# Kernel tuning notes

Hardware: AMD Instinct MI355X
Metric: run time of the kernel (lower is better)

The kernel has to match this reference:

```python
import jax, jax.numpy as jnp
import numpy as np

B, T, F, H, M = 64, 512, 32, 512, 20
O = (F + 2) * M  # (n_features + 2) * num_mixtures = 680


def _lstm_cell(x, h, c, w_ih, w_hh, b_ih, b_hh):
    # torch.nn.LSTMCell: gates ordered [i, f, g, o]
    gates = x @ w_ih.T + h @ w_hh.T + b_ih + b_hh
    i, f, g, o = jnp.split(gates, 4, axis=-1)
    i = jax.nn.sigmoid(i)
    f = jax.nn.sigmoid(f)
    g = jnp.tanh(g)
    o = jax.nn.sigmoid(o)
    c_new = f * c + i * g
    h_new = o * jnp.tanh(c_new)
    return h_new, c_new


def setup_inputs() -> dict:
    key = jax.random.key(0)
    ks = jax.random.split(key, 9)
    s1 = 1.0 / np.sqrt(H)  # torch LSTMCell init: U(-1/sqrt(hidden), 1/sqrt(hidden))
    s2 = 1.0 / np.sqrt(O)
    u = lambda k, shape, s: jax.random.uniform(k, shape, jnp.float32, -s, s)
    return {
        "data": jax.random.normal(ks[0], (B, T * F), jnp.float32),
        "W_ih1": u(ks[1], (4 * H, F), s1),
        "W_hh1": u(ks[2], (4 * H, H), s1),
        "b_ih1": u(ks[3], (4 * H,), s1),
        "b_hh1": u(ks[4], (4 * H,), s1),
        "W_ih2": u(ks[5], (4 * O, H), s2),
        "W_hh2": u(ks[6], (4 * O, O), s2),
        "b_ih2": u(ks[7], (4 * O,), s2),
        "b_hh2": u(ks[8], (4 * O,), s2),
    }


def reference(data, W_ih1, W_hh1, b_ih1, b_hh1, W_ih2, W_hh2, b_ih2, b_hh2):
    n_feat = W_ih1.shape[1]
    hid = W_hh1.shape[1]
    out_dim = W_hh2.shape[1]
    batch = data.shape[0]
    t_steps = data.shape[1] // n_feat
    xs = data.reshape(batch, t_steps, n_feat).transpose(1, 0, 2)  # (T, B, F)

    h1 = jnp.zeros((batch, hid), data.dtype)
    c1 = jnp.zeros((batch, hid), data.dtype)
    h2 = jnp.zeros((batch, out_dim), data.dtype)
    c2 = jnp.zeros((batch, out_dim), data.dtype)

    def step(carry, x_t):
        h1, c1, h2, c2 = carry
        h1, c1 = _lstm_cell(x_t, h1, c1, W_ih1, W_hh1, b_ih1, b_hh1)
        # NOTE: original feeds lstm1's CELL state c1 into lstm2, and collects
        # lstm2's CELL state (`output`) as the per-step output.
        h2, c2 = _lstm_cell(c1, h2, c2, W_ih2, W_hh2, b_ih2, b_hh2)
        return (h1, c1, h2, c2), c2

    _, outs = jax.lax.scan(step, (h1, c1, h2, c2), xs)  # (T, B, O)
    return outs.transpose(1, 0, 2)  # (B, T, O), matches torch.stack(outputs, 1)
```

## Files before the change

kernel.cpp:

```cpp
#include <hip/hip_runtime.h>
#include <math.h>

#define BB 64
#define TT 512
#define FF 32
#define HH 512
#define OO 680

typedef _Float16 half8 __attribute__((ext_vector_type(8)));
typedef float f32x4 __attribute__((ext_vector_type(4)));

#define H1S_OFF 0u
#define C1S_OFF 131072u
#define H2S_OFF 262144u
#define BAR_OFF 442368u
#define MEMSET_BYTES 443648u

#define NBLK 64
#define LDS_BYTES 151552u
#define L2W_OFF 34816u

#define CNT(g) ((g)*32)
#define FLG    256

__device__ __forceinline__ float sigf(float x) { return 1.f / (1.f + expf(-x)); }

__device__ __forceinline__ unsigned long long aload8(const void* p) {
    return __hip_atomic_load((const unsigned long long*)p, __ATOMIC_RELAXED, __HIP_MEMORY_SCOPE_AGENT);
}
__device__ __forceinline__ void astore8(void* p, unsigned long long v) {
    __hip_atomic_store((unsigned long long*)p, v, __ATOMIC_RELAXED, __HIP_MEMORY_SCOPE_AGENT);
}
__device__ __forceinline__ void astore32(unsigned* p, unsigned v) {
    __hip_atomic_store(p, v, __ATOMIC_RELAXED, __HIP_MEMORY_SCOPE_AGENT);
}
__device__ __forceinline__ half8 ld_act(const char* p) {
    union { unsigned long long u[2]; half8 h; } t;
    t.u[0] = aload8(p); t.u[1] = aload8(p + 8);
    return t.h;
}
__device__ __forceinline__ unsigned pack2h(float a, float b) {
    union { _Float16 h[2]; unsigned u; } t;
    t.h[0] = (_Float16)a; t.h[1] = (_Float16)b; return t.u;
}
__device__ __forceinline__ unsigned long long pack4h(float a, float b, float c, float d) {
    union { _Float16 h[4]; unsigned long long u; } t;
    t.h[0] = (_Float16)a; t.h[1] = (_Float16)b; t.h[2] = (_Float16)c; t.h[3] = (_Float16)d;
    return t.u;
}
__device__ __forceinline__ unsigned minFlag(const unsigned* bar) {
    const unsigned long long v0 = aload8(bar + FLG);
    const unsigned long long v1 = aload8(bar + FLG + 2);
    const unsigned long long v2 = aload8(bar + FLG + 4);
    const unsigned long long v3 = aload8(bar + FLG + 6);
    unsigned m = (unsigned)v0, x;
    x = (unsigned)(v0 >> 32); m = x < m ? x : m;
    x = (unsigned)v1;         m = x < m ? x : m;
    x = (unsigned)(v1 >> 32); m = x < m ? x : m;
    x = (unsigned)v2;         m = x < m ? x : m;
    x = (unsigned)(v2 >> 32); m = x < m ? x : m;
    x = (unsigned)v3;         m = x < m ? x : m;
    x = (unsigned)(v3 >> 32); m = x < m ? x : m;
    return m;
}
__device__ __forceinline__ size_t slab_waddr(int cc, int b) {
    return (size_t)((cc >> 5) * 4 + (b >> 4)) * 1024
         + (size_t)((((cc >> 3) & 3) * 16 + (b & 15))) * 16
         + (size_t)(cc & 7) * 2;
}

__global__ __launch_bounds__(256, 1)
void rnn_merged(const float* __restrict__ data,
    const float* __restrict__ Wih1, const float* __restrict__ Whh1,
    const float* __restrict__ bih1, const float* __restrict__ bhh1,
    const float* __restrict__ Wih2, const float* __restrict__ Whh2,
    const float* __restrict__ bih2, const float* __restrict__ bhh2,
    char* __restrict__ wsb, float* __restrict__ out)
{
    extern __shared__ char lds[];
    const int tid = threadIdx.x, wv = tid >> 6, l = tid & 63;
    const int hi = l >> 4, lo = l & 15;
    const int bk = blockIdx.x;
    unsigned* bar = (unsigned*)(wsb + BAR_OFF);
    const int b = wv * 16 + lo;

    for (int u = tid; u < 34 * 256; u += 256) {
        const int tt = u >> 8, w = u & 255;
        const int ks = tt >> 1, q = tt & 1;
        const int ll = w >> 2, jj = w & 3;
        const int fq = q * 16 + (ll & 15);
        const int col = bk * 8 + (fq >> 2);
        const int gate = fq & 3;
        const int grow = gate * HH + col;
        const int k = ks * 32 + (ll >> 4) * 8 + jj * 2;
        const float v0 = (k < FF)     ? Wih1[(size_t)grow * FF + k]     : Whh1[(size_t)grow * HH + k - FF];
        const float v1 = (k + 1 < FF) ? Wih1[(size_t)grow * FF + k + 1] : Whh1[(size_t)grow * HH + k + 1 - FF];
        ((unsigned*)lds)[tt * 256 + w] = pack2h(v0, v1);
    }
    for (int u = tid; u < 114 * 256; u += 256) {
        const int tt = u >> 8, w = u & 255;
        const int ks = tt / 3, q = tt - ks * 3;
        const int ll = w >> 2, jj = w & 3;
        const int fq = q * 16 + (ll & 15);
        const int col = bk * 12 + (fq >> 2);
        const int gate = fq & 3;
        const int k = ks * 32 + (ll >> 4) * 8 + jj * 2;
        float v0 = 0.f, v1 = 0.f;
        if (col < OO) {
            if (k < HH) v0 = Wih2[((size_t)gate * OO + col) * HH + k];
            else if (k < 1192) v0 = Whh2[((size_t)gate * OO + col) * OO + k - HH];
            if (k + 1 < HH) v1 = Wih2[((size_t)gate * OO + col) * HH + k + 1];
            else if (k + 1 < 1192) v1 = Whh2[((size_t)gate * OO + col) * OO + k + 1 - HH];
        }
        ((unsigned*)(lds + L2W_OFF))[tt * 256 + w] = pack2h(v0, v1);
    }
    __syncthreads();

    float bs1[2][4], bs2[3][4];
    #pragma unroll
    for (int q = 0; q < 2; ++q) {
        const int col = bk * 8 + q * 4 + hi;
        #pragma unroll
        for (int g = 0; g < 4; ++g) bs1[q][g] = bih1[g * HH + col] + bhh1[g * HH + col];
    }
    #pragma unroll
    for (int q = 0; q < 3; ++q) {
        const int col = bk * 12 + q * 4 + hi;
        const bool ok = col < OO;
        #pragma unroll
        for (int g = 0; g < 4; ++g) bs2[q][g] = ok ? (bih2[g * OO + col] + bhh2[g * OO + col]) : 0.f;
    }
    float cr1[2] = {0.f, 0.f};
    float cr2[3] = {0.f, 0.f, 0.f};

    for (int s = 0; s <= TT; ++s) {
        const int wr = s & 1, rd = wr ^ 1;
        f32x4 a10 = {0,0,0,0}, a11 = {0,0,0,0};
        if (s < TT) {
            const float* xp = data + (size_t)b * (TT * FF) + (size_t)s * FF + hi * 8;
            const float4 xa = *(const float4*)xp;
            const float4 xb4 = *(const float4*)(xp + 4);
            half8 bx;
            bx[0] = (_Float16)xa.x; bx[1] = (_Float16)xa.y; bx[2] = (_Float16)xa.z; bx[3] = (_Float16)xa.w;
            bx[4] = (_Float16)xb4.x; bx[5] = (_Float16)xb4.y; bx[6] = (_Float16)xb4.z; bx[7] = (_Float16)xb4.w;
            a10 = __builtin_amdgcn_mfma_f32_16x16x32_f16(*(const half8*)(lds + (size_t)l * 16), bx, a10, 0, 0, 0);
            a11 = __builtin_amdgcn_mfma_f32_16x16x32_f16(*(const half8*)(lds + 1024 + (size_t)l * 16), bx, a11, 0, 0, 0);
        }
        if (s > 0) {
            if (tid == 0) { while (minFlag(bar) < (unsigned)s) {} }
            __syncthreads();
        }
        float pend[4]; float* pendP = nullptr;

        if (s < TT) {
            const char* h1p = wsb + H1S_OFF + (size_t)rd * 65536u + (size_t)l * 16;
            half8 bh[16];
            #pragma unroll
            for (int ks = 0; ks < 16; ++ks) bh[ks] = ld_act(h1p + (size_t)(ks * 4 + wv) * 1024);
            #pragma unroll
            for (int ks = 1; ks <= 16; ++ks) {
                a10 = __builtin_amdgcn_mfma_f32_16x16x32_f16(*(const half8*)(lds + (size_t)(ks * 2) * 1024 + (size_t)l * 16), bh[ks - 1], a10, 0, 0, 0);
                a11 = __builtin_amdgcn_mfma_f32_16x16x32_f16(*(const half8*)(lds + (size_t)(ks * 2 + 1) * 1024 + (size_t)l * 16), bh[ks - 1], a11, 0, 0, 0);
            }
            float cn1[2], hn1[2];
            #pragma unroll
            for (int q = 0; q < 2; ++q) {
                const f32x4 a = (q == 0) ? a10 : a11;
                const float ig = sigf(a[0] + bs1[q][0]);
                const float fg = sigf(a[1] + bs1[q][1]);
                const float gg = tanhf(a[2] + bs1[q][2]);
                const float og = sigf(a[3] + bs1[q][3]);
                const float c = fg * cr1[q] + ig * gg;
                cr1[q] = c;
                cn1[q] = c; hn1[q] = og * tanhf(c);
            }
            char* h1w = wsb + H1S_OFF + (size_t)wr * 65536u;
            char* c1w = wsb + C1S_OFF + (size_t)wr * 65536u;
            #pragma unroll
            for (int q = 0; q < 2; ++q) {
                const float h0 = __shfl(hn1[q], lo), h1v = __shfl(hn1[q], 16 + lo);
                const float h2v = __shfl(hn1[q], 32 + lo), h3 = __shfl(hn1[q], 48 + lo);
                const float c0 = __shfl(cn1[q], lo), c1v = __shfl(cn1[q], 16 + lo);
                const float c2v = __shfl(cn1[q], 32 + lo), c3 = __shfl(cn1[q], 48 + lo);
                if (hi == q) {
                    const int cc = bk * 8 + q * 4;
                    const size_t ad = slab_waddr(cc, b);
                    astore8(h1w + ad, pack4h(h0, h1v, h2v, h3));
                    astore8(c1w + ad, pack4h(c0, c1v, c2v, c3));
                }
            }
        }
        if (s >= 1) {
            f32x4 a20 = {0,0,0,0}, a21 = {0,0,0,0}, a22 = {0,0,0,0};
            const char* c1p = wsb + C1S_OFF + (size_t)rd * 65536u + (size_t)l * 16;
            half8 bc[16];
            #pragma unroll
            for (int ks = 0; ks < 16; ++ks) bc[ks] = ld_act(c1p + (size_t)(ks * 4 + wv) * 1024);
            #pragma unroll
            for (int ks = 0; ks < 16; ++ks) {
                const char* at = lds + L2W_OFF + (size_t)(ks * 3) * 1024 + (size_t)l * 16;
                a20 = __builtin_amdgcn_mfma_f32_16x16x32_f16(*(const half8*)(at       ), bc[ks], a20, 0, 0, 0);
                a21 = __builtin_amdgcn_mfma_f32_16x16x32_f16(*(const half8*)(at + 1024), bc[ks], a21, 0, 0, 0);
                a22 = __builtin_amdgcn_mfma_f32_16x16x32_f16(*(const half8*)(at + 2048), bc[ks], a22, 0, 0, 0);
            }
            const char* h2p = wsb + H2S_OFF + (size_t)rd * 90112u + (size_t)l * 16;
            half8 bh2[22];
            #pragma unroll
            for (int kk = 0; kk < 22; ++kk) bh2[kk] = ld_act(h2p + (size_t)(kk * 4 + wv) * 1024);
            #pragma unroll
            for (int kk = 0; kk < 22; ++kk) {
                const char* at = lds + L2W_OFF + (size_t)((16 + kk) * 3) * 1024 + (size_t)l * 16;
                a20 = __builtin_amdgcn_mfma_f32_16x16x32_f16(*(const half8*)(at       ), bh2[kk], a20, 0, 0, 0);
                a21 = __builtin_amdgcn_mfma_f32_16x16x32_f16(*(const half8*)(at + 1024), bh2[kk], a21, 0, 0, 0);
                a22 = __builtin_amdgcn_mfma_f32_16x16x32_f16(*(const half8*)(at + 2048), bh2[kk], a22, 0, 0, 0);
            }
            float cn2[3], hn2[3];
            #pragma unroll
            for (int q = 0; q < 3; ++q) {
                const f32x4 a = (q == 0) ? a20 : (q == 1) ? a21 : a22;
                const float ig = sigf(a[0] + bs2[q][0]);
                const float fg = sigf(a[1] + bs2[q][1]);
                const float gg = tanhf(a[2] + bs2[q][2]);
                const float og = sigf(a[3] + bs2[q][3]);
                const float c = fg * cr2[q] + ig * gg;
                cr2[q] = c;
                cn2[q] = c; hn2[q] = og * tanhf(c);
            }
            char* h2w = wsb + H2S_OFF + (size_t)wr * 90112u;
            #pragma unroll
            for (int q = 0; q < 3; ++q) {
                const float h0 = __shfl(hn2[q], lo), h1v = __shfl(hn2[q], 16 + lo);
                const float h2v = __shfl(hn2[q], 32 + lo), h3 = __shfl(hn2[q], 48 + lo);
                const float c0 = __shfl(cn2[q], lo), c1v = __shfl(cn2[q], 16 + lo);
                const float c2v = __shfl(cn2[q], 32 + lo), c3 = __shfl(cn2[q], 48 + lo);
                if (hi == q) {
                    const int cc = bk * 12 + q * 4;
                    if (cc + 4 <= OO) {
                        astore8(h2w + slab_waddr(cc, b), pack4h(h0, h1v, h2v, h3));
                        pend[0] = c0; pend[1] = c1v; pend[2] = c2v; pend[3] = c3;
                        pendP = out + (size_t)b * (TT * OO) + (size_t)(s - 1) * OO + cc;
                    }
                }
            }
        }
        __syncthreads();
        if (s < TT && tid == 0) {
            const int g = bk & 7;
            const unsigned e = (unsigned)(s + 1);
            const unsigned a = __hip_atomic_fetch_add(bar + CNT(g), 1u, __ATOMIC_RELAXED, __HIP_MEMORY_SCOPE_AGENT);
            if (a == e * 8u - 1u) astore32(bar + FLG + g, e);
        }
        if (pendP) {
            const f32x4 q4 = {pend[0], pend[1], pend[2], pend[3]};
            __builtin_nontemporal_store(q4, (f32x4*)pendP);
        }
    }
}

extern "C" void kernel_launch(void* const* d_in, const int* in_sizes, int n_in,
                              void* d_out, int out_size, void* d_ws, size_t ws_size,
                              hipStream_t stream)
{
    const float* data = (const float*)d_in[0];
    const float* Wih1 = (const float*)d_in[1];
    const float* Whh1 = (const float*)d_in[2];
    const float* bih1 = (const float*)d_in[3];
    const float* bhh1 = (const float*)d_in[4];
    const float* Wih2 = (const float*)d_in[5];
    const float* Whh2 = (const float*)d_in[6];
    const float* bih2 = (const float*)d_in[7];
    const float* bhh2 = (const float*)d_in[8];
    float* out = (float*)d_out;
    char* wsb  = (char*)d_ws;

    hipFuncSetAttribute((const void*)rnn_merged, hipFuncAttributeMaxDynamicSharedMemorySize, (int)LDS_BYTES);
    hipMemsetAsync(wsb, 0, MEMSET_BYTES, stream);
    rnn_merged<<<NBLK, 256, LDS_BYTES, stream>>>(data,
                                                 Wih1, Whh1, bih1, bhh1,
                                                 Wih2, Whh2, bih2, bhh2,
                                                 wsb, out);
}
```

Before: 4.211 ms.

## Replace global barrier wait with per-group flag polling interleaved with MFMA

Instead of thread 0 waiting until all eight group flags reach the step and then a block-wide barrier, every thread now polls the flags and waits only for the group that produced the slab it is about to consume, then issues that slab's loads and MFMAs. Producer groups are remapped to contiguous blocks (bk>>3), so each flag covers a contiguous range of columns. The intent is to overlap the wait with compute on slabs that are already ready and to drop the __syncthreads before the recurrent matmuls. The cost is more polling traffic from all threads and loads issued one at a time instead of batched up front.

```diff
diff --git a/kernel.cpp b/kernel.cpp
--- a/kernel.cpp
+++ b/kernel.cpp
@@ -48,26 +48,41 @@
     t.h[0] = (_Float16)a; t.h[1] = (_Float16)b; t.h[2] = (_Float16)c; t.h[3] = (_Float16)d;
     return t.u;
 }
-__device__ __forceinline__ unsigned minFlag(const unsigned* bar) {
-    const unsigned long long v0 = aload8(bar + FLG);
-    const unsigned long long v1 = aload8(bar + FLG + 2);
-    const unsigned long long v2 = aload8(bar + FLG + 4);
-    const unsigned long long v3 = aload8(bar + FLG + 6);
-    unsigned m = (unsigned)v0, x;
-    x = (unsigned)(v0 >> 32); m = x < m ? x : m;
-    x = (unsigned)v1;         m = x < m ? x : m;
-    x = (unsigned)(v1 >> 32); m = x < m ? x : m;
-    x = (unsigned)v2;         m = x < m ? x : m;
-    x = (unsigned)(v2 >> 32); m = x < m ? x : m;
-    x = (unsigned)v3;         m = x < m ? x : m;
-    x = (unsigned)(v3 >> 32); m = x < m ? x : m;
-    return m;
-}
 __device__ __forceinline__ size_t slab_waddr(int cc, int b) {
     return (size_t)((cc >> 5) * 4 + (b >> 4)) * 1024
          + (size_t)((((cc >> 3) & 3) * 16 + (b & 15))) * 16
          + (size_t)(cc & 7) * 2;
 }
+
+#define POLLG(fcg) \
+    if ((fcg) < tgt) { for (;;) { \
+        const unsigned long long q0 = aload8(bar + FLG);     \
+        const unsigned long long q1 = aload8(bar + FLG + 2); \
+        const unsigned long long q2 = aload8(bar + FLG + 4); \
+        const unsigned long long q3 = aload8(bar + FLG + 6); \
+        fc0 = (unsigned)q0; fc1 = (unsigned)(q0 >> 32);      \
+        fc2 = (unsigned)q1; fc3 = (unsigned)(q1 >> 32);      \
+        fc4 = (unsigned)q2; fc5 = (unsigned)(q2 >> 32);      \
+        fc6 = (unsigned)q3; fc7 = (unsigned)(q3 >> 32);      \
+        if ((fcg) >= tgt) break;                             \
+        __builtin_amdgcn_s_sleep(1); } }
+
+#define MFA(off, B, ACC) ACC = __builtin_amdgcn_mfma_f32_16x16x32_f16(*(const half8*)(lds + (size_t)(off) * 1024u + (size_t)l * 16), (B), ACC, 0, 0, 0)
+#define MFB(off, B, ACC) ACC = __builtin_amdgcn_mfma_f32_16x16x32_f16(*(const half8*)(lds + L2W_OFF + (size_t)(off) * 1024u + (size_t)l * 16), (B), ACC, 0, 0, 0)
+
+#define H1T(t) { const half8 u = ld_act(h1p + (size_t)((t) * 4 + wv) * 1024u); \
+                 MFA(((t) + 1) * 2, u, a10); MFA(((t) + 1) * 2 + 1, u, a11); }
+#define C1T(t) { const half8 u = ld_act(c1p + (size_t)((t) * 4 + wv) * 1024u); \
+                 MFB((t) * 3, u, a20); MFB((t) * 3 + 1, u, a21); MFB((t) * 3 + 2, u, a22); }
+#define H2T(t) { const half8 u = ld_act(h2p + (size_t)((t) * 4 + wv) * 1024u); \
+                 MFB((16 + (t)) * 3, u, a20); MFB((16 + (t)) * 3 + 1, u, a21); MFB((16 + (t)) * 3 + 2, u, a22); }
+
+#define GRP(g, fcg) \
+    POLLG(fcg); \
+    if (s < TT) { H1T(2 * (g)); H1T(2 * (g) + 1); } \
+    if (s >= 1) { C1T(2 * (g)); C1T(2 * (g) + 1); \
+        if ((g) < 7) { H2T(3 * (g)); H2T(3 * (g) + 1); H2T(3 * (g) + 2); } \
+        else         { H2T(21); } }
 
 __global__ __launch_bounds__(256, 1)
 void rnn_merged(const float* __restrict__ data,
@@ -132,10 +147,13 @@
     }
     float cr1[2] = {0.f, 0.f};
     float cr2[3] = {0.f, 0.f, 0.f};
+    unsigned fc0 = 0, fc1 = 0, fc2 = 0, fc3 = 0, fc4 = 0, fc5 = 0, fc6 = 0, fc7 = 0;
 
     for (int s = 0; s <= TT; ++s) {
         const int wr = s & 1, rd = wr ^ 1;
+        const unsigned tgt = (unsigned)s;
         f32x4 a10 = {0,0,0,0}, a11 = {0,0,0,0};
+        f32x4 a20 = {0,0,0,0}, a21 = {0,0,0,0}, a22 = {0,0,0,0};
         if (s < TT) {
             const float* xp = data + (size_t)b * (TT * FF) + (size_t)s * FF + hi * 8;
             const float4 xa = *(const float4*)xp;
@@ -143,25 +161,18 @@
             half8 bx;
             bx[0] = (_Float16)xa.x; bx[1] = (_Float16)xa.y; bx[2] = (_Float16)xa.z; bx[3] = (_Float16)xa.w;
             bx[4] = (_Float16)xb4.x; bx[5] = (_Float16)xb4.y; bx[6] = (_Float16)xb4.z; bx[7] = (_Float16)xb4.w;
-            a10 = __builtin_amdgcn_mfma_f32_16x16x32_f16(*(const half8*)(lds + (size_t)l * 16), bx, a10, 0, 0, 0);
-            a11 = __builtin_amdgcn_mfma_f32_16x16x32_f16(*(const half8*)(lds + 1024 + (size_t)l * 16), bx, a11, 0, 0, 0);
-        }
-        if (s > 0) {
-            if (tid == 0) { while (minFlag(bar) < (unsigned)s) {} }
-            __syncthreads();
-        }
+            MFA(0, bx, a10); MFA(1, bx, a11);
+        }
+        const char* h1p = wsb + H1S_OFF + (size_t)rd * 65536u + (size_t)l * 16;
+        const char* c1p = wsb + C1S_OFF + (size_t)rd * 65536u + (size_t)l * 16;
+        const char* h2p = wsb + H2S_OFF + (size_t)rd * 90112u + (size_t)l * 16;
+
+        GRP(0, fc0); GRP(1, fc1); GRP(2, fc2); GRP(3, fc3);
+        GRP(4, fc4); GRP(5, fc5); GRP(6, fc6); GRP(7, fc7);
+
         float pend[4]; float* pendP = nullptr;
 
         if (s < TT) {
-            const char* h1p = wsb + H1S_OFF + (size_t)rd * 65536u + (size_t)l * 16;
-            half8 bh[16];
-            #pragma unroll
-            for (int ks = 0; ks < 16; ++ks) bh[ks] = ld_act(h1p + (size_t)(ks * 4 + wv) * 1024);
-            #pragma unroll
-            for (int ks = 1; ks <= 16; ++ks) {
-                a10 = __builtin_amdgcn_mfma_f32_16x16x32_f16(*(const half8*)(lds + (size_t)(ks * 2) * 1024 + (size_t)l * 16), bh[ks - 1], a10, 0, 0, 0);
-                a11 = __builtin_amdgcn_mfma_f32_16x16x32_f16(*(const half8*)(lds + (size_t)(ks * 2 + 1) * 1024 + (size_t)l * 16), bh[ks - 1], a11, 0, 0, 0);
-            }
             float cn1[2], hn1[2];
             #pragma unroll
             for (int q = 0; q < 2; ++q) {
@@ -191,29 +202,6 @@
             }
         }
         if (s >= 1) {
-            f32x4 a20 = {0,0,0,0}, a21 = {0,0,0,0}, a22 = {0,0,0,0};
-            const char* c1p = wsb + C1S_OFF + (size_t)rd * 65536u + (size_t)l * 16;
-            half8 bc[16];
-            #pragma unroll
-            for (int ks = 0; ks < 16; ++ks) bc[ks] = ld_act(c1p + (size_t)(ks * 4 + wv) * 1024);
-            #pragma unroll
-            for (int ks = 0; ks < 16; ++ks) {
-                const char* at = lds + L2W_OFF + (size_t)(ks * 3) * 1024 + (size_t)l * 16;
-                a20 = __builtin_amdgcn_mfma_f32_16x16x32_f16(*(const half8*)(at       ), bc[ks], a20, 0, 0, 0);
-                a21 = __builtin_amdgcn_mfma_f32_16x16x32_f16(*(const half8*)(at + 1024), bc[ks], a21, 0, 0, 0);
-                a22 = __builtin_amdgcn_mfma_f32_16x16x32_f16(*(const half8*)(at + 2048), bc[ks], a22, 0, 0, 0);
-            }
-            const char* h2p = wsb + H2S_OFF + (size_t)rd * 90112u + (size_t)l * 16;
-            half8 bh2[22];
-            #pragma unroll
-            for (int kk = 0; kk < 22; ++kk) bh2[kk] = ld_act(h2p + (size_t)(kk * 4 + wv) * 1024);
-            #pragma unroll
-            for (int kk = 0; kk < 22; ++kk) {
-                const char* at = lds + L2W_OFF + (size_t)((16 + kk) * 3) * 1024 + (size_t)l * 16;
-                a20 = __builtin_amdgcn_mfma_f32_16x16x32_f16(*(const half8*)(at       ), bh2[kk], a20, 0, 0, 0);
-                a21 = __builtin_amdgcn_mfma_f32_16x16x32_f16(*(const half8*)(at + 1024), bh2[kk], a21, 0, 0, 0);
-                a22 = __builtin_amdgcn_mfma_f32_16x16x32_f16(*(const half8*)(at + 2048), bh2[kk], a22, 0, 0, 0);
-            }
             float cn2[3], hn2[3];
             #pragma unroll
             for (int q = 0; q < 3; ++q) {
@@ -245,7 +233,7 @@
         }
         __syncthreads();
         if (s < TT && tid == 0) {
-            const int g = bk & 7;
+            const int g = bk >> 3;
             const unsigned e = (unsigned)(s + 1);
             const unsigned a = __hip_atomic_fetch_add(bar + CNT(g), 1u, __ATOMIC_RELAXED, __HIP_MEMORY_SCOPE_AGENT);
             if (a == e * 8u - 1u) astore32(bar + FLG + g, e);
```

Measured after the change: 8.919 ms. 2.12x slower.

## Replace hierarchical atomic-counter grid barrier with per-block flags polled by a wave

Applied to the files above, without the earlier changes.

Replaces the two-level barrier (per-group atomic fetch_add counters plus group flags) with one flag per block that each block stores after its step. A whole wavefront polls all 64 flags in parallel, reduces the minimum with cross-lane shuffles, and sleeps briefly between polls. This drops the atomic read-modify-write from the critical path of every timestep, at the cost of 64 separate loads per poll and relying on relaxed ordering of the flag stores.

```diff
diff --git a/kernel.cpp b/kernel.cpp
--- a/kernel.cpp
+++ b/kernel.cpp
@@ -20,11 +20,11 @@
 #define LDS_BYTES 151552u
 #define L2W_OFF 34816u
 
-#define CNT(g) ((g)*32)
-#define FLG    256
-
 __device__ __forceinline__ float sigf(float x) { return 1.f / (1.f + expf(-x)); }
 
+__device__ __forceinline__ unsigned al32(const unsigned* p) {
+    return __hip_atomic_load(p, __ATOMIC_RELAXED, __HIP_MEMORY_SCOPE_AGENT);
+}
 __device__ __forceinline__ unsigned long long aload8(const void* p) {
     return __hip_atomic_load((const unsigned long long*)p, __ATOMIC_RELAXED, __HIP_MEMORY_SCOPE_AGENT);
 }
@@ -47,21 +47,6 @@
     union { _Float16 h[4]; unsigned long long u; } t;
     t.h[0] = (_Float16)a; t.h[1] = (_Float16)b; t.h[2] = (_Float16)c; t.h[3] = (_Float16)d;
     return t.u;
-}
-__device__ __forceinline__ unsigned minFlag(const unsigned* bar) {
-    const unsigned long long v0 = aload8(bar + FLG);
-    const unsigned long long v1 = aload8(bar + FLG + 2);
-    const unsigned long long v2 = aload8(bar + FLG + 4);
-    const unsigned long long v3 = aload8(bar + FLG + 6);
-    unsigned m = (unsigned)v0, x;
-    x = (unsigned)(v0 >> 32); m = x < m ? x : m;
-    x = (unsigned)v1;         m = x < m ? x : m;
-    x = (unsigned)(v1 >> 32); m = x < m ? x : m;
-    x = (unsigned)v2;         m = x < m ? x : m;
-    x = (unsigned)(v2 >> 32); m = x < m ? x : m;
-    x = (unsigned)v3;         m = x < m ? x : m;
-    x = (unsigned)(v3 >> 32); m = x < m ? x : m;
-    return m;
 }
 __device__ __forceinline__ size_t slab_waddr(int cc, int b) {
     return (size_t)((cc >> 5) * 4 + (b >> 4)) * 1024
@@ -147,7 +132,18 @@
             a11 = __builtin_amdgcn_mfma_f32_16x16x32_f16(*(const half8*)(lds + 1024 + (size_t)l * 16), bx, a11, 0, 0, 0);
         }
         if (s > 0) {
-            if (tid == 0) { while (minFlag(bar) < (unsigned)s) {} }
+            if (wv == 0) {
+                for (;;) {
+                    unsigned v = al32(bar + l);
+                    #pragma unroll
+                    for (int off = 32; off > 0; off >>= 1) {
+                        const unsigned o = __shfl_xor(v, off);
+                        v = (o < v) ? o : v;
+                    }
+                    if (v >= (unsigned)s) break;
+                    __builtin_amdgcn_s_sleep(1);
+                }
+            }
             __syncthreads();
         }
         float pend[4]; float* pendP = nullptr;
@@ -244,12 +240,7 @@
             }
         }
         __syncthreads();
-        if (s < TT && tid == 0) {
-            const int g = bk & 7;
-            const unsigned e = (unsigned)(s + 1);
-            const unsigned a = __hip_atomic_fetch_add(bar + CNT(g), 1u, __ATOMIC_RELAXED, __HIP_MEMORY_SCOPE_AGENT);
-            if (a == e * 8u - 1u) astore32(bar + FLG + g, e);
-        }
+        if (s < TT && tid == 0) astore32(bar + bk, (unsigned)(s + 1));
         if (pendP) {
             const f32x4 q4 = {pend[0], pend[1], pend[2], pend[3]};
             __builtin_nontemporal_store(q4, (f32x4*)pendP);
```

Result: faster. 4.081 ms (-3.1%).
